# Performance work log

Measured on AMD Instinct MI355X. Metric: run time of the kernel, lower is better.

The kernel has to match this reference:

```python
import jax, jax.numpy as jnp
import numpy as np
from jax.scipy.special import logsumexp

# config (matches init_kwargs)
D_IN, D_OUT = 768, 256
P = 2
BLUR = 0.5
SCALING = 0.8
SCALING_FACTOR = 1.0
N_ITERS = 36  # fixed-length eps schedule (clamped at blur), jit-friendly


def setup_inputs() -> dict:
    key = jax.random.key(0)
    k1, k2, k3, k4 = jax.random.split(key, 4)
    d = jax.random.normal(k1, (4096, D_IN), dtype=jnp.float32)
    s1 = jax.random.normal(k2, (1024, D_IN), dtype=jnp.float32)
    s2 = jax.random.normal(k3, (1024, D_IN), dtype=jnp.float32)
    # learned projection parameter (scaled init so projected coords are O(1))
    M = jax.random.normal(k4, (D_IN, D_OUT), dtype=jnp.float32) / np.sqrt(D_IN)
    return {"d": d, "s1": s1, "s2": s2, "M": M}


def _sq_cost(u, v):
    # C[i,j] = ||u_i - v_j||^2 / 2  (geomloss p=2 cost)
    sq = (jnp.sum(u * u, -1)[:, None] + jnp.sum(v * v, -1)[None, :]
          - 2.0 * (u @ v.T))
    return jnp.maximum(sq, 0.0) * 0.5


def _softmin(eps, C, h):
    # -eps * log sum_j exp(h_j - C_ij/eps)   -> shape [C.shape[0]]
    return -eps * logsumexp(h[None, :] - C / eps, axis=1)


def _sinkhorn_divergence(x, y):
    n, m = x.shape[0], y.shape[0]
    a_log = jnp.full((n,), -np.log(n), dtype=x.dtype)  # uniform log-weights
    b_log = jnp.full((m,), -np.log(m), dtype=x.dtype)

    C_xy = _sq_cost(x, y)   # [n, m]
    C_xx = _sq_cost(x, x)   # [n, n]  (debiasing term)
    C_yy = _sq_cost(y, y)   # [m, m]

    # bounding-box diameter of the joint cloud (no grad, like geomloss)
    z = jax.lax.stop_gradient(jnp.concatenate([x, y], axis=0))
    diam = jnp.sqrt(jnp.sum((z.max(0) - z.min(0)) ** 2)) + 1e-6

    # eps-scaling schedule: scale from diameter down to blur, eps = scale^p
    scales = jnp.maximum(BLUR, diam * (SCALING ** jnp.arange(N_ITERS, dtype=x.dtype)))
    eps_list = scales ** P
    eps0 = eps_list[0]
    eps_f = jnp.asarray(BLUR ** P, dtype=x.dtype)

    # init potentials at the largest eps
    f_aa = _softmin(eps0, C_xx, a_log)
    g_bb = _softmin(eps0, C_yy, b_log)
    f_ab = _softmin(eps0, C_xy, b_log)
    g_ab = _softmin(eps0, C_xy.T, a_log)

    @jax.checkpoint
    def step(carry, eps):
        f_aa, g_bb, f_ab, g_ab = carry
        # simultaneous (Jacobi) updates, symmetrized by averaging
        ft = _softmin(eps, C_xy, b_log + g_ab / eps)
        gt = _softmin(eps, C_xy.T, a_log + f_ab / eps)
        f_aa = 0.5 * (f_aa + _softmin(eps, C_xx, a_log + f_aa / eps))
        g_bb = 0.5 * (g_bb + _softmin(eps, C_yy, b_log + g_bb / eps))
        f_ab = 0.5 * (f_ab + ft)
        g_ab = 0.5 * (g_ab + gt)
        return (f_aa, g_bb, f_ab, g_ab), None

    (f_aa, g_bb, f_ab, g_ab), _ = jax.lax.scan(
        step, (f_aa, g_bb, f_ab, g_ab), eps_list)

    # final non-averaged extrapolation at eps = blur^p
    f_ab_n = _softmin(eps_f, C_xy, b_log + g_ab / eps_f)
    g_ab_n = _softmin(eps_f, C_xy.T, a_log + f_ab / eps_f)
    f_aa_n = _softmin(eps_f, C_xx, a_log + f_aa / eps_f)
    g_bb_n = _softmin(eps_f, C_yy, b_log + g_bb / eps_f)

    # debiased divergence with uniform weights: <a, f_ab - f_aa> + <b, g_ab - g_bb>
    return jnp.mean(f_ab_n - f_aa_n) + jnp.mean(g_ab_n - g_bb_n)


def reference(d, s1, s2, M):
    xd = d @ M
    x1 = s1 @ M
    x2 = s2 @ M
    dist1 = _sinkhorn_divergence(xd, x1)
    dist2 = _sinkhorn_divergence(xd, x2)
    return jax.nn.sigmoid(SCALING_FACTOR * (dist2 - dist1))
```

## Files before the change

kernel.cpp:

```cpp
#include <hip/hip_runtime.h>
#include <hip/hip_bf16.h>
#include <math.h>

using ull = unsigned long long;
typedef unsigned short u16x8 __attribute__((ext_vector_type(8)));
typedef __attribute__((ext_vector_type(8))) short bf16x8;
typedef __attribute__((ext_vector_type(4))) float f32x4;

#define ND 4096ull
#define NS 1024ull
#define DOUT 256ull
#define DIN 768ull
#define NIT 36

constexpr ull U_CXX = 0;
constexpr ull U_CXY = U_CXX + ND*ND;
constexpr ull U_CYX = U_CXY + 2*ND*NS;
constexpr ull U_CYY = U_CYX + 2*ND*NS;
constexpr ull U_TOT = U_CYY + 2*NS*NS;
constexpr ull P_XDH = U_TOT;
constexpr ull P_XDM = P_XDH + ND*DOUT;
constexpr ull P_X1H = P_XDM + ND*DOUT;
constexpr ull P_X1M = P_X1H + NS*DOUT;
constexpr ull P_X2H = P_X1M + NS*DOUT;
constexpr ull P_X2M = P_X2H + NS*DOUT;
constexpr ull U_END = P_X2M + NS*DOUT;

constexpr ull O_XD   = U_END / 2;
constexpr ull O_X1   = O_XD + ND*DOUT;
constexpr ull O_X2   = O_X1 + NS*DOUT;
constexpr ull O_MT   = O_X2 + NS*DOUT;
constexpr ull O_ND_  = O_MT + DOUT*DIN;
constexpr ull O_N1   = O_ND_ + ND;
constexpr ull O_N2   = O_N1 + NS;
constexpr ull O_FAB  = O_N2 + NS;
constexpr ull O_GAB  = O_FAB + 4*ND;
constexpr ull O_FAA  = O_GAB + 4*NS;
constexpr ull O_GBB  = O_FAA + 4*ND;
constexpr ull O_FABN = O_GBB + 4*NS;
constexpr ull O_GABN = O_FABN + 2*ND;
constexpr ull O_FAAN = O_GABN + 2*NS;
constexpr ull O_GBBN = O_FAAN + 2*ND;
constexpr ull O_EPS  = O_GBBN + 2*NS;
constexpr ull O_QS   = O_EPS + 2*NIT;
constexpr ull O_DIST = O_QS + 2;
constexpr ull WS_FLOATS = O_DIST + 2;
constexpr ull O_PMIN = O_MT;
constexpr ull O_PMAX = O_MT + 96*256;

constexpr float LOG2E = 1.4426950408889634f;
constexpr float LN2   = 0.69314718055994531f;
constexpr float A_LOG2 = -12.0f;
constexpr float B_LOG2 = -10.0f;

__device__ __forceinline__ float wave_max(float v) {
    #pragma unroll
    for (int o = 32; o; o >>= 1) v = fmaxf(v, __shfl_xor(v, o));
    return v;
}
__device__ __forceinline__ float wave_sum(float v) {
    #pragma unroll
    for (int o = 32; o; o >>= 1) v += __shfl_xor(v, o);
    return v;
}

__device__ __forceinline__ unsigned short f2bf_rn(float x) {
    union { float f; unsigned u; } v; v.f = x;
    const unsigned r = v.u + 0x7FFFu + ((v.u >> 16) & 1u);
    return (unsigned short)(r >> 16);
}
__device__ __forceinline__ float bf2f(unsigned short b) {
    union { unsigned u; float f; } v; v.u = ((unsigned)b) << 16; return v.f;
}

__global__ __launch_bounds__(256)
void transpose_M_k(const float* __restrict__ M, float* __restrict__ Mt)
{
    int idx = blockIdx.x * 256 + threadIdx.x;
    int r = idx >> 8;
    int c = idx & 255;
    Mt[(size_t)c * DIN + r] = M[idx];
}

__global__ __launch_bounds__(256)
void gemm_proj(const float* __restrict__ A, const float* __restrict__ B,
               float* __restrict__ C, int M, int N, int K)
{
    __shared__ __align__(16) float As[16][68];
    __shared__ __align__(16) float Bs[16][68];
    const int m0 = blockIdx.y * 64, n0 = blockIdx.x * 64;
    const int t = threadIdx.x;
    const int lk = t & 15, lr = t >> 4;
    const int tm = t >> 4, tn = t & 15;
    float acc[4][4] = {};
    for (int k0 = 0; k0 < K; k0 += 16) {
        #pragma unroll
        for (int r = 0; r < 4; r++) {
            As[lk][lr + r*16] = A[(size_t)(m0 + lr + r*16) * K + (k0 + lk)];
            Bs[lk][lr + r*16] = B[(size_t)(n0 + lr + r*16) * K + (k0 + lk)];
        }
        __syncthreads();
        #pragma unroll
        for (int k = 0; k < 16; k++) {
            const float4 a4 = *(const float4*)&As[k][tm*4];
            const float4 b4 = *(const float4*)&Bs[k][tn*4];
            const float av[4] = {a4.x, a4.y, a4.z, a4.w};
            const float bv[4] = {b4.x, b4.y, b4.z, b4.w};
            #pragma unroll
            for (int i = 0; i < 4; i++)
                #pragma unroll
                for (int j = 0; j < 4; j++)
                    acc[i][j] = fmaf(av[i], bv[j], acc[i][j]);
        }
        __syncthreads();
    }
    #pragma unroll
    for (int i = 0; i < 4; i++)
        #pragma unroll
        for (int j = 0; j < 4; j++)
            C[(size_t)(m0 + tm*4 + i) * N + (n0 + tn*4 + j)] = acc[i][j];
}

__global__ __launch_bounds__(256)
void pack_bf16_k(const float* __restrict__ X,
                 unsigned short* __restrict__ Phi, unsigned short* __restrict__ Pmi)
{
    const int p = blockIdx.x;
    const int t = threadIdx.x;
    #pragma unroll
    for (int s = t; s < 512; s += 256) {
        const int kb = s >> 6, l = s & 63;
        const int row = p * 16 + (l & 15);
        const int k0 = kb * 32 + ((l >> 4) << 3);
        const float* src = X + (ull)row * DOUT + k0;
        u16x8 hi, mi;
        #pragma unroll
        for (int e = 0; e < 8; e++) {
            const float x = src[e];
            const unsigned short h = f2bf_rn(x);
            hi[e] = h;
            mi[e] = f2bf_rn(x - bf2f(h));
        }
        const ull o = (((ull)p * 8 + kb) * 64 + l) * 8;
        *(u16x8*)&Phi[o] = hi;
        *(u16x8*)&Pmi[o] = mi;
    }
}

__device__ __forceinline__ unsigned int quant16(float c, float s) {
    return __float2uint_rn(fminf(c * s, 65535.0f));
}

__global__ __launch_bounds__(256)
void gemm_cost_mfma(const unsigned short* __restrict__ Ahi, const unsigned short* __restrict__ Ami,
                    const unsigned short* __restrict__ Bhi, const unsigned short* __restrict__ Bmi,
                    unsigned short* __restrict__ C,
                    const float* __restrict__ na, const float* __restrict__ nb,
                    const float* __restrict__ qsp, int N)
{
    const int l = threadIdx.x & 63;
    const int w = threadIdx.x >> 6;
    const int n0 = blockIdx.x * 64, m0 = blockIdx.y * 64;
    const int pA = (m0 >> 4) + w;
    const int pB0 = n0 >> 4;
    f32x4 a0 = {}, a1 = {}, a2 = {}, a3 = {};
    #pragma unroll
    for (int kb = 0; kb < 8; kb++) {
        const ull ao = (((ull)pA * 8 + kb) * 64 + l) * 8;
        const bf16x8 aH = *(const bf16x8*)&Ahi[ao];
        const bf16x8 aM = *(const bf16x8*)&Ami[ao];
        const ull b0o = (((ull)(pB0 + 0) * 8 + kb) * 64 + l) * 8;
        const ull b1o = (((ull)(pB0 + 1) * 8 + kb) * 64 + l) * 8;
        const ull b2o = (((ull)(pB0 + 2) * 8 + kb) * 64 + l) * 8;
        const ull b3o = (((ull)(pB0 + 3) * 8 + kb) * 64 + l) * 8;
        bf16x8 bH, bM;
        bH = *(const bf16x8*)&Bhi[b0o]; bM = *(const bf16x8*)&Bmi[b0o];
        a0 = __builtin_amdgcn_mfma_f32_16x16x32_bf16(aH, bH, a0, 0, 0, 0);
        a0 = __builtin_amdgcn_mfma_f32_16x16x32_bf16(aH, bM, a0, 0, 0, 0);
        a0 = __builtin_amdgcn_mfma_f32_16x16x32_bf16(aM, bH, a0, 0, 0, 0);
        bH = *(const bf16x8*)&Bhi[b1o]; bM = *(const bf16x8*)&Bmi[b1o];
        a1 = __builtin_amdgcn_mfma_f32_16x16x32_bf16(aH, bH, a1, 0, 0, 0);
        a1 = __builtin_amdgcn_mfma_f32_16x16x32_bf16(aH, bM, a1, 0, 0, 0);
        a1 = __builtin_amdgcn_mfma_f32_16x16x32_bf16(aM, bH, a1, 0, 0, 0);
        bH = *(const bf16x8*)&Bhi[b2o]; bM = *(const bf16x8*)&Bmi[b2o];
        a2 = __builtin_amdgcn_mfma_f32_16x16x32_bf16(aH, bH, a2, 0, 0, 0);
        a2 = __builtin_amdgcn_mfma_f32_16x16x32_bf16(aH, bM, a2, 0, 0, 0);
        a2 = __builtin_amdgcn_mfma_f32_16x16x32_bf16(aM, bH, a2, 0, 0, 0);
        bH = *(const bf16x8*)&Bhi[b3o]; bM = *(const bf16x8*)&Bmi[b3o];
        a3 = __builtin_amdgcn_mfma_f32_16x16x32_bf16(aH, bH, a3, 0, 0, 0);
        a3 = __builtin_amdgcn_mfma_f32_16x16x32_bf16(aH, bM, a3, 0, 0, 0);
        a3 = __builtin_amdgcn_mfma_f32_16x16x32_bf16(aM, bH, a3, 0, 0, 0);
    }
    const float s = qsp[0];
    const int row0 = m0 + w * 16 + ((l >> 4) << 2);
    const int col = l & 15;
    float nar[4];
    #pragma unroll
    for (int r = 0; r < 4; r++) nar[r] = na[row0 + r];
    const float nb0 = nb[n0 + col];
    const float nb1 = nb[n0 + 16 + col];
    const float nb2 = nb[n0 + 32 + col];
    const float nb3 = nb[n0 + 48 + col];
    #pragma unroll
    for (int r = 0; r < 4; r++) {
        const ull rowb = (ull)(row0 + r) * N + n0;
        C[rowb + col]      = (unsigned short)quant16(0.5f * fmaxf(nar[r] + nb0 - 2.0f * a0[r], 0.0f), s);
        C[rowb + 16 + col] = (unsigned short)quant16(0.5f * fmaxf(nar[r] + nb1 - 2.0f * a1[r], 0.0f), s);
        C[rowb + 32 + col] = (unsigned short)quant16(0.5f * fmaxf(nar[r] + nb2 - 2.0f * a2[r], 0.0f), s);
        C[rowb + 48 + col] = (unsigned short)quant16(0.5f * fmaxf(nar[r] + nb3 - 2.0f * a3[r], 0.0f), s);
    }
}

__global__ __launch_bounds__(256)
void row_norm(const float* __restrict__ x, float* __restrict__ o)
{
    const int i = blockIdx.x;
    const float v = x[(size_t)i * DOUT + threadIdx.x];
    float s = wave_sum(v * v);
    __shared__ float red[4];
    const int wid = threadIdx.x >> 6, lane = threadIdx.x & 63;
    if (lane == 0) red[wid] = s;
    __syncthreads();
    if (threadIdx.x == 0) o[i] = red[0] + red[1] + red[2] + red[3];
}

__global__ __launch_bounds__(256)
void colminmax_k(const float* __restrict__ xd, const float* __restrict__ x1,
                 const float* __restrict__ x2, float* __restrict__ ws)
{
    const int b = blockIdx.x, c = threadIdx.x;
    const float* src; int r0;
    if (b < 64)      { src = xd; r0 = b * 64; }
    else if (b < 80) { src = x1; r0 = (b - 64) * 64; }
    else             { src = x2; r0 = (b - 80) * 64; }
    float mn = 3.4e38f, mx = -3.4e38f;
    for (int r = 0; r < 64; r++) {
        const float v = src[(size_t)(r0 + r) * DOUT + c];
        mn = fminf(mn, v); mx = fmaxf(mx, v);
    }
    ws[O_PMIN + (ull)b * 256 + c] = mn;
    ws[O_PMAX + (ull)b * 256 + c] = mx;
}

__global__ __launch_bounds__(256)
void eps_k(float* __restrict__ ws)
{
    const int c = threadIdx.x;
    const float* pmin = ws + O_PMIN;
    const float* pmax = ws + O_PMAX;
    float mnd = 3.4e38f, mxd = -3.4e38f;
    float mn1 = 3.4e38f, mx1 = -3.4e38f;
    float mn2 = 3.4e38f, mx2 = -3.4e38f;
    for (int b = 0;  b < 64; b++) { mnd = fminf(mnd, pmin[b*256+c]); mxd = fmaxf(mxd, pmax[b*256+c]); }
    for (int b = 64; b < 80; b++) { mn1 = fminf(mn1, pmin[b*256+c]); mx1 = fmaxf(mx1, pmax[b*256+c]); }
    for (int b = 80; b < 96; b++) { mn2 = fminf(mn2, pmin[b*256+c]); mx2 = fmaxf(mx2, pmax[b*256+c]); }
    const float d1 = fmaxf(mxd, mx1) - fminf(mnd, mn1);
    const float d2 = fmaxf(mxd, mx2) - fminf(mnd, mn2);
    float s1 = wave_sum(d1 * d1);
    float s2 = wave_sum(d2 * d2);
    __shared__ float r1[4], r2[4];
    const int wid = c >> 6, lane = c & 63;
    if (lane == 0) { r1[wid] = s1; r2[wid] = s2; }
    __syncthreads();
    if (c == 0) {
        const float d1s = r1[0]+r1[1]+r1[2]+r1[3];
        const float d2s = r2[0]+r2[1]+r2[2]+r2[3];
        const float cb = 0.5f * fmaxf(d1s, d2s) * 1.02f + 1.0f;
        ws[O_QS]     = 65535.0f / cb;
        ws[O_QS + 1] = cb / 65535.0f;
    }
    if (c < 2 * NIT) {
        const int div = c / NIT, tt = c % NIT;
        const float ss = div ? (r2[0]+r2[1]+r2[2]+r2[3]) : (r1[0]+r1[1]+r1[2]+r1[3]);
        const float diam = sqrtf(ss) + 1e-6f;
        const float sc = fmaxf(0.5f, diam * powf(0.8f, (float)tt));
        ws[O_EPS + (ull)div * NIT + tt] = sc * sc;
    }
}

template<int NC>
__device__ __forceinline__ void softmin_row_q(
    const unsigned short* __restrict__ Crow, const float* __restrict__ hvec,
    float hc2, float eps, float qs,
    const float* __restrict__ selfv, float* __restrict__ outp,
    int row, int phase, int lane)
{
    const float ie2 = LOG2E / eps;
    const float qsc = -qs * ie2;
    const u16x8* Q8 = (const u16x8*)Crow;
    const float4* H4 = (const float4*)hvec;
    float v[NC * 8];
    #pragma unroll
    for (int c = 0; c < NC; c++) {
        const u16x8 q = Q8[c * 64 + lane];
        if (hvec) {
            const float4 ha = H4[c * 128 + lane * 2];
            const float4 hb = H4[c * 128 + lane * 2 + 1];
            const float hv[8] = {ha.x, ha.y, ha.z, ha.w, hb.x, hb.y, hb.z, hb.w};
            #pragma unroll
            for (int e = 0; e < 8; e++)
                v[c*8 + e] = fmaf((float)q[e], qsc, fmaf(hv[e], ie2, hc2));
        } else {
            #pragma unroll
            for (int e = 0; e < 8; e++)
                v[c*8 + e] = fmaf((float)q[e], qsc, hc2);
        }
    }
    float m = v[0];
    #pragma unroll
    for (int k = 1; k < NC * 8; k++) m = fmaxf(m, v[k]);
    m = wave_max(m);
    float s = 0.0f;
    #pragma unroll
    for (int k = 0; k < NC * 8; k++) s += exp2f(v[k] - m);
    s = wave_sum(s);
    if (lane == 0) {
        float res = -eps * LN2 * (m + log2f(s));
        if (phase == 1) res = 0.5f * (selfv[row] + res);
        outp[row] = res;
    }
}

__global__ __launch_bounds__(256)
void sinkhorn_phase(float* __restrict__ ws, int phase, int t)
{
    const unsigned short* uq = (const unsigned short*)ws;
    const int wid = threadIdx.x >> 6, lane = threadIdx.x & 63;
    const int w = blockIdx.x * 4 + wid;
    const float qs = ws[O_QS + 1];
    int rb, wb;
    if (phase == 0) { rb = 0; wb = 0; }
    else { rb = t & 1; wb = rb ^ 1; }

    if (w < 8192) {
        const int div = w >> 12, i = w & 4095;
        const float eps = (phase == 2) ? 0.25f : ws[O_EPS + (ull)div * NIT + t];
        const unsigned short* Crow = uq + U_CXY + (ull)div * ND * NS + (ull)i * NS;
        const float* gab_r = ws + O_GAB + ((ull)div * 2 + rb) * NS;
        const float* fab_r = ws + O_FAB + ((ull)div * 2 + rb) * ND;
        float* outp = (phase == 2) ? (ws + O_FABN + (ull)div * ND)
                                   : (ws + O_FAB + ((ull)div * 2 + wb) * ND);
        softmin_row_q<2>(Crow, phase ? gab_r : nullptr, B_LOG2, eps, qs, fab_r, outp, i, phase, lane);
    } else if (w < 10240) {
        const int q = w - 8192, div = q >> 10, j = q & 1023;
        const float eps = (phase == 2) ? 0.25f : ws[O_EPS + (ull)div * NIT + t];
        const unsigned short* Crow = uq + U_CYX + (ull)div * ND * NS + (ull)j * ND;
        const float* fab_r = ws + O_FAB + ((ull)div * 2 + rb) * ND;
        const float* gab_r = ws + O_GAB + ((ull)div * 2 + rb) * NS;
        float* outp = (phase == 2) ? (ws + O_GABN + (ull)div * NS)
                                   : (ws + O_GAB + ((ull)div * 2 + wb) * NS);
        softmin_row_q<8>(Crow, phase ? fab_r : nullptr, A_LOG2, eps, qs, gab_r, outp, j, phase, lane);
    } else if (w < 14336) {
        const int i = w - 10240;
        const float eps0 = (phase == 2) ? 0.25f : ws[O_EPS + t];
        const float eps1 = (phase == 2) ? 0.25f : ws[O_EPS + NIT + t];
        const unsigned short* Crow = uq + U_CXX + (ull)i * ND;
        const float* faa_r0 = ws + O_FAA + (ull)rb * ND;
        const float* faa_r1 = ws + O_FAA + (2ull + rb) * ND;
        float* out0 = (phase == 2) ? (ws + O_FAAN)      : (ws + O_FAA + (ull)wb * ND);
        float* out1 = (phase == 2) ? (ws + O_FAAN + ND) : (ws + O_FAA + (2ull + wb) * ND);
        softmin_row_q<8>(Crow, phase ? faa_r0 : nullptr, A_LOG2, eps0, qs, faa_r0, out0, i, phase, lane);
        softmin_row_q<8>(Crow, phase ? faa_r1 : nullptr, A_LOG2, eps1, qs, faa_r1, out1, i, phase, lane);
    } else {
        const int q = w - 14336, div = q >> 10, i = q & 1023;
        const float eps = (phase == 2) ? 0.25f : ws[O_EPS + (ull)div * NIT + t];
        const unsigned short* Crow = uq + U_CYY + (ull)div * NS * NS + (ull)i * NS;
        const float* gbb_r = ws + O_GBB + ((ull)div * 2 + rb) * NS;
        float* outp = (phase == 2) ? (ws + O_GBBN + (ull)div * NS)
                                   : (ws + O_GBB + ((ull)div * 2 + wb) * NS);
        softmin_row_q<2>(Crow, phase ? gbb_r : nullptr, B_LOG2, eps, qs, gbb_r, outp, i, phase, lane);
    }
}

__global__ __launch_bounds__(256)
void reduce_dist(float* __restrict__ ws)
{
    const int d = blockIdx.x;
    const int tix = threadIdx.x;
    float s = 0.0f;
    #pragma unroll
    for (int k = 0; k < 16; k++) {
        const int i = tix + k * 256;
        s += (ws[O_FABN + (ull)d * ND + i] - ws[O_FAAN + (ull)d * ND + i]) * (1.0f / 4096.0f);
    }
    #pragma unroll
    for (int k = 0; k < 4; k++) {
        const int j = tix + k * 256;
        s += (ws[O_GABN + (ull)d * NS + j] - ws[O_GBBN + (ull)d * NS + j]) * (1.0f / 1024.0f);
    }
    s = wave_sum(s);
    __shared__ float red[4];
    const int wid = tix >> 6, lane = tix & 63;
    if (lane == 0) red[wid] = s;
    __syncthreads();
    if (tix == 0) ws[O_DIST + d] = red[0] + red[1] + red[2] + red[3];
}

__global__ void finalize_k(const float* __restrict__ ws, float* __restrict__ out)
{
    const float x = ws[O_DIST + 1] - ws[O_DIST + 0];
    out[0] = 1.0f / (1.0f + expf(-x));
}

extern "C" void kernel_launch(void* const* d_in, const int* in_sizes, int n_in,
                              void* d_out, int out_size, void* d_ws, size_t ws_size,
                              hipStream_t stream)
{
    if (ws_size < WS_FLOATS * sizeof(float)) return;

    const float* dmat = (const float*)d_in[0];
    const float* s1   = (const float*)d_in[1];
    const float* s2   = (const float*)d_in[2];
    const float* M    = (const float*)d_in[3];
    float* ws  = (float*)d_ws;
    float* out = (float*)d_out;
    unsigned short* uq = (unsigned short*)d_ws;

    float* Mt = ws + O_MT;
    float* xd = ws + O_XD;
    float* x1 = ws + O_X1;
    float* x2 = ws + O_X2;

    transpose_M_k<<<768, 256, 0, stream>>>(M, Mt);
    gemm_proj<<<dim3(4, 64), 256, 0, stream>>>(dmat, Mt, xd, 4096, 256, 768);
    gemm_proj<<<dim3(4, 16), 256, 0, stream>>>(s1,   Mt, x1, 1024, 256, 768);
    gemm_proj<<<dim3(4, 16), 256, 0, stream>>>(s2,   Mt, x2, 1024, 256, 768);
    row_norm<<<4096, 256, 0, stream>>>(xd, ws + O_ND_);
    row_norm<<<1024, 256, 0, stream>>>(x1, ws + O_N1);
    row_norm<<<1024, 256, 0, stream>>>(x2, ws + O_N2);
    colminmax_k<<<96, 256, 0, stream>>>(xd, x1, x2, ws);
    eps_k<<<1, 256, 0, stream>>>(ws);
    pack_bf16_k<<<256, 256, 0, stream>>>(xd, uq + P_XDH, uq + P_XDM);
    pack_bf16_k<<<64,  256, 0, stream>>>(x1, uq + P_X1H, uq + P_X1M);
    pack_bf16_k<<<64,  256, 0, stream>>>(x2, uq + P_X2H, uq + P_X2M);
    const float* qsp = ws + O_QS;
    const float* nd_ = ws + O_ND_;
    const float* n1  = ws + O_N1;
    const float* n2  = ws + O_N2;
    gemm_cost_mfma<<<dim3(64, 64), 256, 0, stream>>>(uq+P_XDH, uq+P_XDM, uq+P_XDH, uq+P_XDM, uq + U_CXX,           nd_, nd_, qsp, 4096);
    gemm_cost_mfma<<<dim3(16, 64), 256, 0, stream>>>(uq+P_XDH, uq+P_XDM, uq+P_X1H, uq+P_X1M, uq + U_CXY,           nd_, n1,  qsp, 1024);
    gemm_cost_mfma<<<dim3(64, 16), 256, 0, stream>>>(uq+P_X1H, uq+P_X1M, uq+P_XDH, uq+P_XDM, uq + U_CYX,           n1,  nd_, qsp, 4096);
    gemm_cost_mfma<<<dim3(16, 64), 256, 0, stream>>>(uq+P_XDH, uq+P_XDM, uq+P_X2H, uq+P_X2M, uq + U_CXY + ND*NS,   nd_, n2,  qsp, 1024);
    gemm_cost_mfma<<<dim3(64, 16), 256, 0, stream>>>(uq+P_X2H, uq+P_X2M, uq+P_XDH, uq+P_XDM, uq + U_CYX + ND*NS,   n2,  nd_, qsp, 4096);
    gemm_cost_mfma<<<dim3(16, 16), 256, 0, stream>>>(uq+P_X1H, uq+P_X1M, uq+P_X1H, uq+P_X1M, uq + U_CYY,           n1,  n1,  qsp, 1024);
    gemm_cost_mfma<<<dim3(16, 16), 256, 0, stream>>>(uq+P_X2H, uq+P_X2M, uq+P_X2H, uq+P_X2M, uq + U_CYY + NS*NS,   n2,  n2,  qsp, 1024);
    sinkhorn_phase<<<4096, 256, 0, stream>>>(ws, 0, 0);
    for (int t = 0; t < NIT; t++)
        sinkhorn_phase<<<4096, 256, 0, stream>>>(ws, 1, t);
    sinkhorn_phase<<<4096, 256, 0, stream>>>(ws, 2, 36);
    reduce_dist<<<2, 256, 0, stream>>>(ws);
    finalize_k<<<1, 1, 0, stream>>>(ws, out);
}
```

Before: 1.445 ms.

## Use online softmax for long rows and fuse dual-eps Cxx softmin

Rows with 8 chunks (Cyx and Cxx) now use a streaming max/sum instead of holding 64 values per lane, which lowers register pressure, and launch bounds now request 8 blocks per CU. The two Cxx softmins for both divergences are fused into one pass, so the quantized Cxx row is loaded and converted once instead of twice. Short rows get split partial-sum accumulators to shorten the dependency chain. The online form adds an extra exp2 rescale per chunk.

Measured after the change: 2.299 ms. 59.1% more time.

```diff
diff --git a/kernel.cpp b/kernel.cpp
--- a/kernel.cpp
+++ b/kernel.cpp
@@ -278,8 +278,13 @@
     }
 }
 
+__device__ __forceinline__ float tmax8(const float* v) {
+    return fmaxf(fmaxf(fmaxf(v[0],v[1]),fmaxf(v[2],v[3])),
+                 fmaxf(fmaxf(v[4],v[5]),fmaxf(v[6],v[7])));
+}
+
 template<int NC>
-__device__ __forceinline__ void softmin_row_q(
+__device__ __forceinline__ void softmin_flat(
     const unsigned short* __restrict__ Crow, const float* __restrict__ hvec,
     float hc2, float eps, float qs,
     const float* __restrict__ selfv, float* __restrict__ outp,
@@ -287,15 +292,14 @@
 {
     const float ie2 = LOG2E / eps;
     const float qsc = -qs * ie2;
-    const u16x8* Q8 = (const u16x8*)Crow;
-    const float4* H4 = (const float4*)hvec;
     float v[NC * 8];
     #pragma unroll
     for (int c = 0; c < NC; c++) {
-        const u16x8 q = Q8[c * 64 + lane];
+        const int off = c * 512 + lane * 8;
+        const u16x8 q = *(const u16x8*)&Crow[off];
         if (hvec) {
-            const float4 ha = H4[c * 128 + lane * 2];
-            const float4 hb = H4[c * 128 + lane * 2 + 1];
+            const float4 ha = *(const float4*)&hvec[off];
+            const float4 hb = *(const float4*)&hvec[off + 4];
             const float hv[8] = {ha.x, ha.y, ha.z, ha.w, hb.x, hb.y, hb.z, hb.w};
             #pragma unroll
             for (int e = 0; e < 8; e++)
@@ -310,10 +314,10 @@
     #pragma unroll
     for (int k = 1; k < NC * 8; k++) m = fmaxf(m, v[k]);
     m = wave_max(m);
-    float s = 0.0f;
-    #pragma unroll
-    for (int k = 0; k < NC * 8; k++) s += exp2f(v[k] - m);
-    s = wave_sum(s);
+    float sa[4] = {0.0f, 0.0f, 0.0f, 0.0f};
+    #pragma unroll
+    for (int k = 0; k < NC * 8; k++) sa[k & 3] += exp2f(v[k] - m);
+    float s = wave_sum((sa[0] + sa[1]) + (sa[2] + sa[3]));
     if (lane == 0) {
         float res = -eps * LN2 * (m + log2f(s));
         if (phase == 1) res = 0.5f * (selfv[row] + res);
@@ -321,7 +325,138 @@
     }
 }
 
-__global__ __launch_bounds__(256)
+template<int NC>
+__device__ __forceinline__ void softmin_online(
+    const unsigned short* __restrict__ Crow, const float* __restrict__ hvec,
+    float hc2, float eps, float qs,
+    const float* __restrict__ selfv, float* __restrict__ outp,
+    int row, int phase, int lane)
+{
+    const float ie2 = LOG2E / eps;
+    const float qsc = -qs * ie2;
+    float m = -1e30f, s = 0.0f;
+    #pragma unroll
+    for (int c = 0; c < NC; c++) {
+        const int off = c * 512 + lane * 8;
+        const u16x8 q = *(const u16x8*)&Crow[off];
+        float v[8];
+        if (hvec) {
+            const float4 ha = *(const float4*)&hvec[off];
+            const float4 hb = *(const float4*)&hvec[off + 4];
+            v[0] = fmaf((float)q[0], qsc, fmaf(ha.x, ie2, hc2));
+            v[1] = fmaf((float)q[1], qsc, fmaf(ha.y, ie2, hc2));
+            v[2] = fmaf((float)q[2], qsc, fmaf(ha.z, ie2, hc2));
+            v[3] = fmaf((float)q[3], qsc, fmaf(ha.w, ie2, hc2));
+            v[4] = fmaf((float)q[4], qsc, fmaf(hb.x, ie2, hc2));
+            v[5] = fmaf((float)q[5], qsc, fmaf(hb.y, ie2, hc2));
+            v[6] = fmaf((float)q[6], qsc, fmaf(hb.z, ie2, hc2));
+            v[7] = fmaf((float)q[7], qsc, fmaf(hb.w, ie2, hc2));
+        } else {
+            #pragma unroll
+            for (int e = 0; e < 8; e++) v[e] = fmaf((float)q[e], qsc, hc2);
+        }
+        const float cm = tmax8(v);
+        const float mn = fmaxf(m, cm);
+        float p0 = exp2f(v[0]-mn) + exp2f(v[1]-mn);
+        float p1 = exp2f(v[2]-mn) + exp2f(v[3]-mn);
+        float p2 = exp2f(v[4]-mn) + exp2f(v[5]-mn);
+        float p3 = exp2f(v[6]-mn) + exp2f(v[7]-mn);
+        s = fmaf(s, exp2f(m - mn), (p0 + p1) + (p2 + p3));
+        m = mn;
+    }
+    const float mt = wave_max(m);
+    const float st = wave_sum(s * exp2f(m - mt));
+    if (lane == 0) {
+        float res = -eps * LN2 * (mt + log2f(st));
+        if (phase == 1) res = 0.5f * (selfv[row] + res);
+        outp[row] = res;
+    }
+}
+
+__device__ __forceinline__ void softmin_faa_online(
+    const unsigned short* __restrict__ Crow,
+    const float* __restrict__ h0, const float* __restrict__ h1,
+    float eps0, float eps1, float qs,
+    float* __restrict__ out0, float* __restrict__ out1,
+    int row, int phase, int lane)
+{
+    const float ie0 = LOG2E / eps0, ie1 = LOG2E / eps1;
+    const float qs0 = -qs * ie0, qs1 = -qs * ie1;
+    float m0 = -1e30f, s0 = 0.0f, m1 = -1e30f, s1 = 0.0f;
+    #pragma unroll
+    for (int c = 0; c < 8; c++) {
+        const int off = c * 512 + lane * 8;
+        const u16x8 q = *(const u16x8*)&Crow[off];
+        float cq[8];
+        #pragma unroll
+        for (int e = 0; e < 8; e++) cq[e] = (float)q[e];
+        float v[8];
+        if (phase) {
+            const float4 a = *(const float4*)&h0[off];
+            const float4 b = *(const float4*)&h0[off + 4];
+            v[0] = fmaf(cq[0], qs0, fmaf(a.x, ie0, A_LOG2));
+            v[1] = fmaf(cq[1], qs0, fmaf(a.y, ie0, A_LOG2));
+            v[2] = fmaf(cq[2], qs0, fmaf(a.z, ie0, A_LOG2));
+            v[3] = fmaf(cq[3], qs0, fmaf(a.w, ie0, A_LOG2));
+            v[4] = fmaf(cq[4], qs0, fmaf(b.x, ie0, A_LOG2));
+            v[5] = fmaf(cq[5], qs0, fmaf(b.y, ie0, A_LOG2));
+            v[6] = fmaf(cq[6], qs0, fmaf(b.z, ie0, A_LOG2));
+            v[7] = fmaf(cq[7], qs0, fmaf(b.w, ie0, A_LOG2));
+        } else {
+            #pragma unroll
+            for (int e = 0; e < 8; e++) v[e] = fmaf(cq[e], qs0, A_LOG2);
+        }
+        {
+            const float mn = fmaxf(m0, tmax8(v));
+            float p0 = exp2f(v[0]-mn) + exp2f(v[1]-mn);
+            float p1 = exp2f(v[2]-mn) + exp2f(v[3]-mn);
+            float p2 = exp2f(v[4]-mn) + exp2f(v[5]-mn);
+            float p3 = exp2f(v[6]-mn) + exp2f(v[7]-mn);
+            s0 = fmaf(s0, exp2f(m0 - mn), (p0 + p1) + (p2 + p3));
+            m0 = mn;
+        }
+        if (phase) {
+            const float4 a = *(const float4*)&h1[off];
+            const float4 b = *(const float4*)&h1[off + 4];
+            v[0] = fmaf(cq[0], qs1, fmaf(a.x, ie1, A_LOG2));
+            v[1] = fmaf(cq[1], qs1, fmaf(a.y, ie1, A_LOG2));
+            v[2] = fmaf(cq[2], qs1, fmaf(a.z, ie1, A_LOG2));
+            v[3] = fmaf(cq[3], qs1, fmaf(a.w, ie1, A_LOG2));
+            v[4] = fmaf(cq[4], qs1, fmaf(b.x, ie1, A_LOG2));
+            v[5] = fmaf(cq[5], qs1, fmaf(b.y, ie1, A_LOG2));
+            v[6] = fmaf(cq[6], qs1, fmaf(b.z, ie1, A_LOG2));
+            v[7] = fmaf(cq[7], qs1, fmaf(b.w, ie1, A_LOG2));
+        } else {
+            #pragma unroll
+            for (int e = 0; e < 8; e++) v[e] = fmaf(cq[e], qs1, A_LOG2);
+        }
+        {
+            const float mn = fmaxf(m1, tmax8(v));
+            float p0 = exp2f(v[0]-mn) + exp2f(v[1]-mn);
+            float p1 = exp2f(v[2]-mn) + exp2f(v[3]-mn);
+            float p2 = exp2f(v[4]-mn) + exp2f(v[5]-mn);
+            float p3 = exp2f(v[6]-mn) + exp2f(v[7]-mn);
+            s1 = fmaf(s1, exp2f(m1 - mn), (p0 + p1) + (p2 + p3));
+            m1 = mn;
+        }
+    }
+    float mt = wave_max(m0);
+    float st = wave_sum(s0 * exp2f(m0 - mt));
+    if (lane == 0) {
+        float res = -eps0 * LN2 * (mt + log2f(st));
+        if (phase == 1) res = 0.5f * (h0[row] + res);
+        out0[row] = res;
+    }
+    mt = wave_max(m1);
+    st = wave_sum(s1 * exp2f(m1 - mt));
+    if (lane == 0) {
+        float res = -eps1 * LN2 * (mt + log2f(st));
+        if (phase == 1) res = 0.5f * (h1[row] + res);
+        out1[row] = res;
+    }
+}
+
+__global__ __launch_bounds__(256, 8)
 void sinkhorn_phase(float* __restrict__ ws, int phase, int t)
 {
     const unsigned short* uq = (const unsigned short*)ws;
@@ -340,7 +475,7 @@
         const float* fab_r = ws + O_FAB + ((ull)div * 2 + rb) * ND;
         float* outp = (phase == 2) ? (ws + O_FABN + (ull)div * ND)
                                    : (ws + O_FAB + ((ull)div * 2 + wb) * ND);
-        softmin_row_q<2>(Crow, phase ? gab_r : nullptr, B_LOG2, eps, qs, fab_r, outp, i, phase, lane);
+        softmin_flat<2>(Crow, phase ? gab_r : nullptr, B_LOG2, eps, qs, fab_r, outp, i, phase, lane);
     } else if (w < 10240) {
         const int q = w - 8192, div = q >> 10, j = q & 1023;
         const float eps = (phase == 2) ? 0.25f : ws[O_EPS + (ull)div * NIT + t];
@@ -349,7 +484,7 @@
         const float* gab_r = ws + O_GAB + ((ull)div * 2 + rb) * NS;
         float* outp = (phase == 2) ? (ws + O_GABN + (ull)div * NS)
                                    : (ws + O_GAB + ((ull)div * 2 + wb) * NS);
-        softmin_row_q<8>(Crow, phase ? fab_r : nullptr, A_LOG2, eps, qs, gab_r, outp, j, phase, lane);
+        softmin_online<8>(Crow, phase ? fab_r : nullptr, A_LOG2, eps, qs, gab_r, outp, j, phase, lane);
     } else if (w < 14336) {
         const int i = w - 10240;
         const float eps0 = (phase == 2) ? 0.25f : ws[O_EPS + t];
@@ -359,8 +494,7 @@
         const float* faa_r1 = ws + O_FAA + (2ull + rb) * ND;
         float* out0 = (phase == 2) ? (ws + O_FAAN)      : (ws + O_FAA + (ull)wb * ND);
         float* out1 = (phase == 2) ? (ws + O_FAAN + ND) : (ws + O_FAA + (2ull + wb) * ND);
-        softmin_row_q<8>(Crow, phase ? faa_r0 : nullptr, A_LOG2, eps0, qs, faa_r0, out0, i, phase, lane);
-        softmin_row_q<8>(Crow, phase ? faa_r1 : nullptr, A_LOG2, eps1, qs, faa_r1, out1, i, phase, lane);
+        softmin_faa_online(Crow, faa_r0, faa_r1, eps0, eps1, qs, out0, out1, i, phase, lane);
     } else {
         const int q = w - 14336, div = q >> 10, i = q & 1023;
         const float eps = (phase == 2) ? 0.25f : ws[O_EPS + (ull)div * NIT + t];
@@ -368,7 +502,7 @@
         const float* gbb_r = ws + O_GBB + ((ull)div * 2 + rb) * NS;
         float* outp = (phase == 2) ? (ws + O_GBBN + (ull)div * NS)
                                    : (ws + O_GBB + ((ull)div * 2 + wb) * NS);
-        softmin_row_q<2>(Crow, phase ? gbb_r : nullptr, B_LOG2, eps, qs, gbb_r, outp, i, phase, lane);
+        softmin_flat<2>(Crow, phase ? gbb_r : nullptr, B_LOG2, eps, qs, gbb_r, outp, i, phase, lane);
     }
 }
 
```

## Move input projection to split-bf16 MFMA and enlarge cost GEMM tiles

Applied to the files above, without the earlier changes.

Replaces the scalar-FMA shared-memory projection GEMM with an MFMA kernel using a hi/mid bf16 split of the inputs and the transposed projection matrix, which adds pack kernels and extra workspace. Cost-matrix GEMM tiles grow from 64x64 to 128x64 per block, so each A fragment feeds two row groups and B loads are reused more. The projection was FP32 FMA-bound, and the aim is to run it on matrix cores at close to FP32 accuracy. The added pack passes and larger workspace cost some memory traffic, and the three-term bf16 split keeps some error compared with full FP32.

Measured after the change: 1.431 ms. Within noise of the previous version (-1.0%).

```diff
diff --git a/kernel.cpp b/kernel.cpp
--- a/kernel.cpp
+++ b/kernel.cpp
@@ -24,7 +24,15 @@
 constexpr ull P_X1M = P_X1H + NS*DOUT;
 constexpr ull P_X2H = P_X1M + NS*DOUT;
 constexpr ull P_X2M = P_X2H + NS*DOUT;
-constexpr ull U_END = P_X2M + NS*DOUT;
+constexpr ull P_DH  = P_X2M + NS*DOUT;
+constexpr ull P_DM  = P_DH + ND*DIN;
+constexpr ull P_S1H = P_DM + ND*DIN;
+constexpr ull P_S1M = P_S1H + NS*DIN;
+constexpr ull P_S2H = P_S1M + NS*DIN;
+constexpr ull P_S2M = P_S2H + NS*DIN;
+constexpr ull P_MTH = P_S2M + NS*DIN;
+constexpr ull P_MTM = P_MTH + DOUT*DIN;
+constexpr ull U_END = P_MTM + DOUT*DIN;
 
 constexpr ull O_XD   = U_END / 2;
 constexpr ull O_X1   = O_XD + ND*DOUT;
@@ -83,56 +91,18 @@
 }
 
 __global__ __launch_bounds__(256)
-void gemm_proj(const float* __restrict__ A, const float* __restrict__ B,
-               float* __restrict__ C, int M, int N, int K)
-{
-    __shared__ __align__(16) float As[16][68];
-    __shared__ __align__(16) float Bs[16][68];
-    const int m0 = blockIdx.y * 64, n0 = blockIdx.x * 64;
-    const int t = threadIdx.x;
-    const int lk = t & 15, lr = t >> 4;
-    const int tm = t >> 4, tn = t & 15;
-    float acc[4][4] = {};
-    for (int k0 = 0; k0 < K; k0 += 16) {
-        #pragma unroll
-        for (int r = 0; r < 4; r++) {
-            As[lk][lr + r*16] = A[(size_t)(m0 + lr + r*16) * K + (k0 + lk)];
-            Bs[lk][lr + r*16] = B[(size_t)(n0 + lr + r*16) * K + (k0 + lk)];
-        }
-        __syncthreads();
-        #pragma unroll
-        for (int k = 0; k < 16; k++) {
-            const float4 a4 = *(const float4*)&As[k][tm*4];
-            const float4 b4 = *(const float4*)&Bs[k][tn*4];
-            const float av[4] = {a4.x, a4.y, a4.z, a4.w};
-            const float bv[4] = {b4.x, b4.y, b4.z, b4.w};
-            #pragma unroll
-            for (int i = 0; i < 4; i++)
-                #pragma unroll
-                for (int j = 0; j < 4; j++)
-                    acc[i][j] = fmaf(av[i], bv[j], acc[i][j]);
-        }
-        __syncthreads();
-    }
-    #pragma unroll
-    for (int i = 0; i < 4; i++)
-        #pragma unroll
-        for (int j = 0; j < 4; j++)
-            C[(size_t)(m0 + tm*4 + i) * N + (n0 + tn*4 + j)] = acc[i][j];
-}
-
-__global__ __launch_bounds__(256)
-void pack_bf16_k(const float* __restrict__ X,
-                 unsigned short* __restrict__ Phi, unsigned short* __restrict__ Pmi)
+void pack_bf16_gen(const float* __restrict__ X,
+                   unsigned short* __restrict__ Phi, unsigned short* __restrict__ Pmi,
+                   int KB)
 {
     const int p = blockIdx.x;
     const int t = threadIdx.x;
-    #pragma unroll
-    for (int s = t; s < 512; s += 256) {
+    const int K = KB * 32;
+    for (int s = t; s < KB * 64; s += 256) {
         const int kb = s >> 6, l = s & 63;
         const int row = p * 16 + (l & 15);
         const int k0 = kb * 32 + ((l >> 4) << 3);
-        const float* src = X + (ull)row * DOUT + k0;
+        const float* src = X + (ull)row * K + k0;
         u16x8 hi, mi;
         #pragma unroll
         for (int e = 0; e < 8; e++) {
@@ -141,9 +111,54 @@
             hi[e] = h;
             mi[e] = f2bf_rn(x - bf2f(h));
         }
-        const ull o = (((ull)p * 8 + kb) * 64 + l) * 8;
+        const ull o = (((ull)p * KB + kb) * 64 + l) * 8;
         *(u16x8*)&Phi[o] = hi;
         *(u16x8*)&Pmi[o] = mi;
+    }
+}
+
+__global__ __launch_bounds__(256)
+void gemm_proj_mfma(const unsigned short* __restrict__ Ahi, const unsigned short* __restrict__ Ami,
+                    const unsigned short* __restrict__ Bhi, const unsigned short* __restrict__ Bmi,
+                    float* __restrict__ C, int N, int KB)
+{
+    const int l = threadIdx.x & 63;
+    const int w = threadIdx.x >> 6;
+    const int n0 = blockIdx.x * 64, m0 = blockIdx.y * 128;
+    const int pA0 = (m0 >> 4) + w * 2;
+    const int pB0 = n0 >> 4;
+    f32x4 acc[2][4] = {};
+    for (int kb = 0; kb < KB; kb++) {
+        const ull a0o = (((ull)(pA0 + 0) * KB + kb) * 64 + l) * 8;
+        const ull a1o = (((ull)(pA0 + 1) * KB + kb) * 64 + l) * 8;
+        const bf16x8 aH0 = *(const bf16x8*)&Ahi[a0o];
+        const bf16x8 aM0 = *(const bf16x8*)&Ami[a0o];
+        const bf16x8 aH1 = *(const bf16x8*)&Ahi[a1o];
+        const bf16x8 aM1 = *(const bf16x8*)&Ami[a1o];
+        #pragma unroll
+        for (int j = 0; j < 4; j++) {
+            const ull bo = (((ull)(pB0 + j) * KB + kb) * 64 + l) * 8;
+            const bf16x8 bH = *(const bf16x8*)&Bhi[bo];
+            const bf16x8 bM = *(const bf16x8*)&Bmi[bo];
+            acc[0][j] = __builtin_amdgcn_mfma_f32_16x16x32_bf16(aH0, bH, acc[0][j], 0, 0, 0);
+            acc[0][j] = __builtin_amdgcn_mfma_f32_16x16x32_bf16(aH0, bM, acc[0][j], 0, 0, 0);
+            acc[0][j] = __builtin_amdgcn_mfma_f32_16x16x32_bf16(aM0, bH, acc[0][j], 0, 0, 0);
+            acc[1][j] = __builtin_amdgcn_mfma_f32_16x16x32_bf16(aH1, bH, acc[1][j], 0, 0, 0);
+            acc[1][j] = __builtin_amdgcn_mfma_f32_16x16x32_bf16(aH1, bM, acc[1][j], 0, 0, 0);
+            acc[1][j] = __builtin_amdgcn_mfma_f32_16x16x32_bf16(aM1, bH, acc[1][j], 0, 0, 0);
+        }
+    }
+    const int col = l & 15;
+    #pragma unroll
+    for (int i = 0; i < 2; i++) {
+        const int row0 = m0 + w * 32 + i * 16 + ((l >> 4) << 2);
+        #pragma unroll
+        for (int r = 0; r < 4; r++) {
+            const ull rowb = (ull)(row0 + r) * N + n0;
+            #pragma unroll
+            for (int j = 0; j < 4; j++)
+                C[rowb + j * 16 + col] = acc[i][j][r];
+        }
     }
 }
 
@@ -160,54 +175,48 @@
 {
     const int l = threadIdx.x & 63;
     const int w = threadIdx.x >> 6;
-    const int n0 = blockIdx.x * 64, m0 = blockIdx.y * 64;
-    const int pA = (m0 >> 4) + w;
+    const int n0 = blockIdx.x * 64, m0 = blockIdx.y * 128;
+    const int pA0 = (m0 >> 4) + w * 2;
     const int pB0 = n0 >> 4;
-    f32x4 a0 = {}, a1 = {}, a2 = {}, a3 = {};
+    f32x4 acc[2][4] = {};
     #pragma unroll
     for (int kb = 0; kb < 8; kb++) {
-        const ull ao = (((ull)pA * 8 + kb) * 64 + l) * 8;
-        const bf16x8 aH = *(const bf16x8*)&Ahi[ao];
-        const bf16x8 aM = *(const bf16x8*)&Ami[ao];
-        const ull b0o = (((ull)(pB0 + 0) * 8 + kb) * 64 + l) * 8;
-        const ull b1o = (((ull)(pB0 + 1) * 8 + kb) * 64 + l) * 8;
-        const ull b2o = (((ull)(pB0 + 2) * 8 + kb) * 64 + l) * 8;
-        const ull b3o = (((ull)(pB0 + 3) * 8 + kb) * 64 + l) * 8;
-        bf16x8 bH, bM;
-        bH = *(const bf16x8*)&Bhi[b0o]; bM = *(const bf16x8*)&Bmi[b0o];
-        a0 = __builtin_amdgcn_mfma_f32_16x16x32_bf16(aH, bH, a0, 0, 0, 0);
-        a0 = __builtin_amdgcn_mfma_f32_16x16x32_bf16(aH, bM, a0, 0, 0, 0);
-        a0 = __builtin_amdgcn_mfma_f32_16x16x32_bf16(aM, bH, a0, 0, 0, 0);
-        bH = *(const bf16x8*)&Bhi[b1o]; bM = *(const bf16x8*)&Bmi[b1o];
-        a1 = __builtin_amdgcn_mfma_f32_16x16x32_bf16(aH, bH, a1, 0, 0, 0);
-        a1 = __builtin_amdgcn_mfma_f32_16x16x32_bf16(aH, bM, a1, 0, 0, 0);
-        a1 = __builtin_amdgcn_mfma_f32_16x16x32_bf16(aM, bH, a1, 0, 0, 0);
-        bH = *(const bf16x8*)&Bhi[b2o]; bM = *(const bf16x8*)&Bmi[b2o];
-        a2 = __builtin_amdgcn_mfma_f32_16x16x32_bf16(aH, bH, a2, 0, 0, 0);
-        a2 = __builtin_amdgcn_mfma_f32_16x16x32_bf16(aH, bM, a2, 0, 0, 0);
-        a2 = __builtin_amdgcn_mfma_f32_16x16x32_bf16(aM, bH, a2, 0, 0, 0);
-        bH = *(const bf16x8*)&Bhi[b3o]; bM = *(const bf16x8*)&Bmi[b3o];
-        a3 = __builtin_amdgcn_mfma_f32_16x16x32_bf16(aH, bH, a3, 0, 0, 0);
-        a3 = __builtin_amdgcn_mfma_f32_16x16x32_bf16(aH, bM, a3, 0, 0, 0);
-        a3 = __builtin_amdgcn_mfma_f32_16x16x32_bf16(aM, bH, a3, 0, 0, 0);
+        const ull a0o = (((ull)(pA0 + 0) * 8 + kb) * 64 + l) * 8;
+        const ull a1o = (((ull)(pA0 + 1) * 8 + kb) * 64 + l) * 8;
+        const bf16x8 aH0 = *(const bf16x8*)&Ahi[a0o];
+        const bf16x8 aM0 = *(const bf16x8*)&Ami[a0o];
+        const bf16x8 aH1 = *(const bf16x8*)&Ahi[a1o];
+        const bf16x8 aM1 = *(const bf16x8*)&Ami[a1o];
+        #pragma unroll
+        for (int j = 0; j < 4; j++) {
+            const ull bo = (((ull)(pB0 + j) * 8 + kb) * 64 + l) * 8;
+            const bf16x8 bH = *(const bf16x8*)&Bhi[bo];
+            const bf16x8 bM = *(const bf16x8*)&Bmi[bo];
+            acc[0][j] = __builtin_amdgcn_mfma_f32_16x16x32_bf16(aH0, bH, acc[0][j], 0, 0, 0);
+            acc[0][j] = __builtin_amdgcn_mfma_f32_16x16x32_bf16(aH0, bM, acc[0][j], 0, 0, 0);
+            acc[0][j] = __builtin_amdgcn_mfma_f32_16x16x32_bf16(aM0, bH, acc[0][j], 0, 0, 0);
+            acc[1][j] = __builtin_amdgcn_mfma_f32_16x16x32_bf16(aH1, bH, acc[1][j], 0, 0, 0);
+            acc[1][j] = __builtin_amdgcn_mfma_f32_16x16x32_bf16(aH1, bM, acc[1][j], 0, 0, 0);
+            acc[1][j] = __builtin_amdgcn_mfma_f32_16x16x32_bf16(aM1, bH, acc[1][j], 0, 0, 0);
+        }
     }
     const float s = qsp[0];
-    const int row0 = m0 + w * 16 + ((l >> 4) << 2);
     const int col = l & 15;
-    float nar[4];
-    #pragma unroll
-    for (int r = 0; r < 4; r++) nar[r] = na[row0 + r];
-    const float nb0 = nb[n0 + col];
-    const float nb1 = nb[n0 + 16 + col];
-    const float nb2 = nb[n0 + 32 + col];
-    const float nb3 = nb[n0 + 48 + col];
-    #pragma unroll
-    for (int r = 0; r < 4; r++) {
-        const ull rowb = (ull)(row0 + r) * N + n0;
-        C[rowb + col]      = (unsigned short)quant16(0.5f * fmaxf(nar[r] + nb0 - 2.0f * a0[r], 0.0f), s);
-        C[rowb + 16 + col] = (unsigned short)quant16(0.5f * fmaxf(nar[r] + nb1 - 2.0f * a1[r], 0.0f), s);
-        C[rowb + 32 + col] = (unsigned short)quant16(0.5f * fmaxf(nar[r] + nb2 - 2.0f * a2[r], 0.0f), s);
-        C[rowb + 48 + col] = (unsigned short)quant16(0.5f * fmaxf(nar[r] + nb3 - 2.0f * a3[r], 0.0f), s);
+    float nbj[4];
+    #pragma unroll
+    for (int j = 0; j < 4; j++) nbj[j] = nb[n0 + j * 16 + col];
+    #pragma unroll
+    for (int i = 0; i < 2; i++) {
+        const int row0 = m0 + w * 32 + i * 16 + ((l >> 4) << 2);
+        #pragma unroll
+        for (int r = 0; r < 4; r++) {
+            const float nar = na[row0 + r];
+            const ull rowb = (ull)(row0 + r) * N + n0;
+            #pragma unroll
+            for (int j = 0; j < 4; j++)
+                C[rowb + j * 16 + col] =
+                    (unsigned short)quant16(0.5f * fmaxf(nar + nbj[j] - 2.0f * acc[i][j][r], 0.0f), s);
+        }
     }
 }
 
@@ -422,28 +431,32 @@
     float* x2 = ws + O_X2;
 
     transpose_M_k<<<768, 256, 0, stream>>>(M, Mt);
-    gemm_proj<<<dim3(4, 64), 256, 0, stream>>>(dmat, Mt, xd, 4096, 256, 768);
-    gemm_proj<<<dim3(4, 16), 256, 0, stream>>>(s1,   Mt, x1, 1024, 256, 768);
-    gemm_proj<<<dim3(4, 16), 256, 0, stream>>>(s2,   Mt, x2, 1024, 256, 768);
+    pack_bf16_gen<<<256, 256, 0, stream>>>(dmat, uq + P_DH,  uq + P_DM,  24);
+    pack_bf16_gen<<<64,  256, 0, stream>>>(s1,   uq + P_S1H, uq + P_S1M, 24);
+    pack_bf16_gen<<<64,  256, 0, stream>>>(s2,   uq + P_S2H, uq + P_S2M, 24);
+    pack_bf16_gen<<<16,  256, 0, stream>>>(Mt,   uq + P_MTH, uq + P_MTM, 24);
+    gemm_proj_mfma<<<dim3(4, 32), 256, 0, stream>>>(uq+P_DH,  uq+P_DM,  uq+P_MTH, uq+P_MTM, xd, 256, 24);
+    gemm_proj_mfma<<<dim3(4, 8),  256, 0, stream>>>(uq+P_S1H, uq+P_S1M, uq+P_MTH, uq+P_MTM, x1, 256, 24);
+    gemm_proj_mfma<<<dim3(4, 8),  256, 0, stream>>>(uq+P_S2H, uq+P_S2M, uq+P_MTH, uq+P_MTM, x2, 256, 24);
     row_norm<<<4096, 256, 0, stream>>>(xd, ws + O_ND_);
     row_norm<<<1024, 256, 0, stream>>>(x1, ws + O_N1);
     row_norm<<<1024, 256, 0, stream>>>(x2, ws + O_N2);
     colminmax_k<<<96, 256, 0, stream>>>(xd, x1, x2, ws);
     eps_k<<<1, 256, 0, stream>>>(ws);
-    pack_bf16_k<<<256, 256, 0, stream>>>(xd, uq + P_XDH, uq + P_XDM);
-    pack_bf16_k<<<64,  256, 0, stream>>>(x1, uq + P_X1H, uq + P_X1M);
-    pack_bf16_k<<<64,  256, 0, stream>>>(x2, uq + P_X2H, uq + P_X2M);
+    pack_bf16_gen<<<256, 256, 0, stream>>>(xd, uq + P_XDH, uq + P_XDM, 8);
+    pack_bf16_gen<<<64,  256, 0, stream>>>(x1, uq + P_X1H, uq + P_X1M, 8);
+    pack_bf16_gen<<<64,  256, 0, stream>>>(x2, uq + P_X2H, uq + P_X2M, 8);
     const float* qsp = ws + O_QS;
     const float* nd_ = ws + O_ND_;
     const float* n1  = ws + O_N1;
     const float* n2  = ws + O_N2;
-    gemm_cost_mfma<<<dim3(64, 64), 256, 0, stream>>>(uq+P_XDH, uq+P_XDM, uq+P_XDH, uq+P_XDM, uq + U_CXX,           nd_, nd_, qsp, 4096);
-    gemm_cost_mfma<<<dim3(16, 64), 256, 0, stream>>>(uq+P_XDH, uq+P_XDM, uq+P_X1H, uq+P_X1M, uq + U_CXY,           nd_, n1,  qsp, 1024);
-    gemm_cost_mfma<<<dim3(64, 16), 256, 0, stream>>>(uq+P_X1H, uq+P_X1M, uq+P_XDH, uq+P_XDM, uq + U_CYX,           n1,  nd_, qsp, 4096);
-    gemm_cost_mfma<<<dim3(16, 64), 256, 0, stream>>>(uq+P_XDH, uq+P_XDM, uq+P_X2H, uq+P_X2M, uq + U_CXY + ND*NS,   nd_, n2,  qsp, 1024);
-    gemm_cost_mfma<<<dim3(64, 16), 256, 0, stream>>>(uq+P_X2H, uq+P_X2M, uq+P_XDH, uq+P_XDM, uq + U_CYX + ND*NS,   n2,  nd_, qsp, 4096);
-    gemm_cost_mfma<<<dim3(16, 16), 256, 0, stream>>>(uq+P_X1H, uq+P_X1M, uq+P_X1H, uq+P_X1M, uq + U_CYY,           n1,  n1,  qsp, 1024);
-    gemm_cost_mfma<<<dim3(16, 16), 256, 0, stream>>>(uq+P_X2H, uq+P_X2M, uq+P_X2H, uq+P_X2M, uq + U_CYY + NS*NS,   n2,  n2,  qsp, 1024);
+    gemm_cost_mfma<<<dim3(64, 32), 256, 0, stream>>>(uq+P_XDH, uq+P_XDM, uq+P_XDH, uq+P_XDM, uq + U_CXX,         nd_, nd_, qsp, 4096);
+    gemm_cost_mfma<<<dim3(16, 32), 256, 0, stream>>>(uq+P_XDH, uq+P_XDM, uq+P_X1H, uq+P_X1M, uq + U_CXY,         nd_, n1,  qsp, 1024);
+    gemm_cost_mfma<<<dim3(64, 8),  256, 0, stream>>>(uq+P_X1H, uq+P_X1M, uq+P_XDH, uq+P_XDM, uq + U_CYX,         n1,  nd_, qsp, 4096);
+    gemm_cost_mfma<<<dim3(16, 32), 256, 0, stream>>>(uq+P_XDH, uq+P_XDM, uq+P_X2H, uq+P_X2M, uq + U_CXY + ND*NS, nd_, n2,  qsp, 1024);
+    gemm_cost_mfma<<<dim3(64, 8),  256, 0, stream>>>(uq+P_X2H, uq+P_X2M, uq+P_XDH, uq+P_XDM, uq + U_CYX + ND*NS, n2,  nd_, qsp, 4096);
+    gemm_cost_mfma<<<dim3(16, 8),  256, 0, stream>>>(uq+P_X1H, uq+P_X1M, uq+P_X1H, uq+P_X1M, uq + U_CYY,         n1,  n1,  qsp, 1024);
+    gemm_cost_mfma<<<dim3(16, 8),  256, 0, stream>>>(uq+P_X2H, uq+P_X2M, uq+P_X2H, uq+P_X2M, uq + U_CYY + NS*NS, n2,  n2,  qsp, 1024);
     sinkhorn_phase<<<4096, 256, 0, stream>>>(ws, 0, 0);
     for (int t = 0; t < NIT; t++)
         sinkhorn_phase<<<4096, 256, 0, stream>>>(ws, 1, t);
```
